# Kernel optimization log

Hardware: AMD Instinct MI355X
Metric: run time of the kernel (lower is better)

## Reference

```python
import jax, jax.numpy as jnp
import numpy as np
from jax import lax

B, T, D, H, S = 256, 512, 256, 512, 8


def setup_inputs() -> dict:
    key = jax.random.key(0)
    ks = jax.random.split(key, 8)
    bound = 1.0 / np.sqrt(H)  # torch LSTMCell/Linear default init scale
    u = lambda k_, shp: jax.random.uniform(k_, shp, jnp.float32, -bound, bound)
    _input = jax.random.normal(ks[0], (B, T, D), jnp.float32)
    h0 = jax.random.normal(ks[1], (B, H), jnp.float32)
    c0 = jax.random.normal(ks[2], (B, H), jnp.float32)
    W_ih = u(ks[3], (4 * H, D))
    W_hh = u(ks[4], (4 * H, H))
    b_ih = u(ks[5], (4 * H,))
    b_hh = u(ks[6], (4 * H,))
    W_lin = u(ks[7], (D, H))
    b_lin = jnp.zeros((D,), jnp.float32)
    # random skip weights per module logic: w1~Bern; w2=1 if w1==0 else Bern; first S steps (1,0)
    rng = np.random.default_rng(0)
    w1 = rng.integers(0, 2, T)
    w2 = np.where(w1 == 0, 1, rng.integers(0, 2, T))
    w1[:S] = 1
    w2[:S] = 0
    return {
        "_input": _input, "h0": h0, "c0": c0,
        "W_ih": W_ih, "W_hh": W_hh, "b_ih": b_ih, "b_hh": b_hh,
        "W_lin": W_lin, "b_lin": b_lin,
        "w1": jnp.asarray(w1, jnp.int32), "w2": jnp.asarray(w2, jnp.int32),
        "time_steps": T, "skip_size": S,
    }


def _lstm_cell(x, h, c, W_ih, W_hh, b_ih, b_hh):
    gates = x @ W_ih.T + b_ih + h @ W_hh.T + b_hh  # [B, 4H]
    i, f, g, o = jnp.split(gates, 4, axis=-1)
    i, f, o = jax.nn.sigmoid(i), jax.nn.sigmoid(f), jax.nn.sigmoid(o)
    c_new = f * c + i * jnp.tanh(g)
    h_new = o * jnp.tanh(c_new)
    return h_new, c_new


def reference(_input, h0, c0, W_ih, W_hh, b_ih, b_hh, W_lin, b_lin, w1, w2, time_steps, skip_size):
    # decoder-mode RSCN: feed previous linear(h) as next input
    buf_h = jnp.repeat(h0[None], skip_size, axis=0)  # FIFO queue as ring buffer [S,B,H]
    buf_c = jnp.repeat(c0[None], skip_size, axis=0)

    def step(carry, xs):
        h_feed, h, c, bh, bc = carry
        w1t, w2t, t = xs
        h_new, c_new = _lstm_cell(h_feed, h, c, W_ih, W_hh, b_ih, b_hh)
        pos = t % skip_size
        skip_h, skip_c = bh[pos], bc[pos]  # queue.get() (oldest)
        bh = bh.at[pos].set(h_new)          # queue.put(new)
        bc = bc.at[pos].set(c_new)
        a = w1t.astype(h_new.dtype)
        b = w2t.astype(h_new.dtype)
        norm = 1.0 / (a + b)
        comb_h = (a * h_new + b * jnp.tanh(skip_h)) * norm
        comb_c = (a * c_new + b * jnp.tanh(skip_c)) * norm
        out = comb_h @ W_lin.T + b_lin  # [B, D]
        return (out, comb_h, comb_c, bh, bc), out

    xs = (w1[:time_steps], w2[:time_steps], jnp.arange(time_steps))
    carry0 = (_input[:, 0, :], h0, c0, buf_h, buf_c)
    (_, h_fin, c_fin, _, _), outs = lax.scan(step, carry0, xs)
    return outs.transpose(1, 0, 2), h_fin, c_fin  # [B,T,D], final (h, c)
```

## Files before the change

### kernel.cpp

```cpp
#include <hip/hip_runtime.h>
#include <math.h>

#define BB 256
#define TT 512
#define DD 256
#define HH 512
#define SS 8
#define G4H 2048
#define BH (BB*HH)
#define OUT_BASE ((size_t)BB*TT*DD)
#define NGRP 16
#define GR 16
#define XSLOT_U32 4096
#define FSTRIDE 16

typedef _Float16 f16;
typedef __attribute__((ext_vector_type(8))) _Float16 f16x8;
typedef __attribute__((ext_vector_type(4))) float    f32x4;

__device__ __forceinline__ float sigm(float x) { return 1.f / (1.f + __expf(-x)); }
__device__ __forceinline__ float ftanh(float x) {
  x = fminf(15.f, fmaxf(-15.f, x));
  float e = __expf(-2.f * x);
  return (1.f - e) / (1.f + e);
}


__global__ __launch_bounds__(256) void prep_wbig16(
    const float* __restrict__ W_ih, const float* __restrict__ W_hh,
    const float* __restrict__ W_lin, f16* __restrict__ Wbig16)
{
  __shared__ float As[64][20];
  __shared__ float Bs[16][68];
  const int n0 = blockIdx.x * 64;
  const int j0 = blockIdx.y * 64;
  const int tid = threadIdx.x;
  const int tn = tid >> 4, tj = tid & 15;
  float acc[4][4] = {};
  for (int k0 = 0; k0 < DD; k0 += 16) {
    { int r = tid >> 2, c = (tid & 3) * 4;
      *(float4*)&As[r][c] = *(const float4*)&W_ih[(size_t)(n0 + r) * DD + k0 + c]; }
    { int r = tid >> 4, c = (tid & 15) * 4;
      *(float4*)&Bs[r][c] = *(const float4*)&W_lin[(size_t)(k0 + r) * HH + j0 + c]; }
    __syncthreads();
    #pragma unroll
    for (int k = 0; k < 16; ++k) {
      float a[4], bv[4];
      #pragma unroll
      for (int i = 0; i < 4; ++i) a[i] = As[tn*4+i][k];
      #pragma unroll
      for (int m = 0; m < 4; ++m) bv[m] = Bs[k][tj*4+m];
      #pragma unroll
      for (int i = 0; i < 4; ++i)
        #pragma unroll
        for (int m = 0; m < 4; ++m)
          acc[i][m] = fmaf(a[i], bv[m], acc[i][m]);
    }
    __syncthreads();
  }
  #pragma unroll
  for (int i = 0; i < 4; ++i) {
    int n = n0 + tn*4 + i;
    #pragma unroll
    for (int m = 0; m < 4; ++m) {
      int j = j0 + tj*4 + m;
      Wbig16[(size_t)n*HH + j] = (f16)(acc[i][m] + W_hh[(size_t)n*HH + j]);
    }
  }
}

__global__ void prep_bias(const float* __restrict__ b_ih, const float* __restrict__ b_hh,
                          const float* __restrict__ W_ih, const float* __restrict__ b_lin,
                          float* __restrict__ bias0, float* __restrict__ bias1)
{
  int n = blockIdx.x * 256 + threadIdx.x;
  float s = b_ih[n] + b_hh[n];
  float d = 0.f;
  for (int k = 0; k < DD; ++k) d = fmaf(W_ih[(size_t)n*DD + k], b_lin[k], d);
  bias0[n] = s;
  bias1[n] = s + d;
}

#define NIH (G4H*DD)
#define NHH (G4H*HH)
__global__ void prep_cvtw(const float* __restrict__ W_ih, const float* __restrict__ W_hh,
                          const float* __restrict__ W_lin,
                          f16* __restrict__ Wih16, f16* __restrict__ Whh16,
                          f16* __restrict__ Wlin16)
{
  int e = blockIdx.x * 256 + threadIdx.x;
  if (e < NIH) Wih16[e] = (f16)W_ih[e];
  else if (e < NIH + NHH) Whh16[e - NIH] = (f16)W_hh[e - NIH];
  else Wlin16[e - NIH - NHH] = (f16)W_lin[e - NIH - NHH];
}

__global__ void prep_init(const float* __restrict__ x0, const float* __restrict__ h0,
                          const float* __restrict__ c0,
                          const int* __restrict__ w1, const int* __restrict__ w2,
                          float* __restrict__ bh, float* __restrict__ bc,
                          f16* __restrict__ x0hi, f16* __restrict__ x0lo,
                          f16* __restrict__ h0hi, f16* __restrict__ h0lo,
                          float4* __restrict__ stepc,
                          int* __restrict__ flags)
{
  int e = blockIdx.x * 256 + threadIdx.x;
  int r = e & (BH - 1);
  bh[e] = h0[r];
  bc[e] = c0[r];
  if (e < BH) {
    float v = h0[e];
    f16 hi = (f16)v;
    h0hi[e] = hi;
    h0lo[e] = (f16)(v - (float)hi);
  }
  if (e < BB*DD) {
    int b = e >> 8, d = e & 255;
    float v = x0[(size_t)b*(TT*DD) + d];
    f16 hi = (f16)v;
    x0hi[e] = hi;
    x0lo[e] = (f16)(v - (float)hi);
  }
  if (e < TT) {
    float a1 = (float)w1[e], a2 = (float)w2[e];
    stepc[e] = make_float4(a1, a2, 1.f / (a1 + a2), 0.f);
  }
  if (e < 4096) flags[e] = 0;
}


__device__ __forceinline__ void stageG(const unsigned* __restrict__ Xs,
                                       f16* lds, int tid) {
  const int lane = tid & 63;
  const int wv = tid >> 6;
  #pragma unroll
  for (int i = 0; i < 2; ++i) {
    int r = wv * 2 + i;
    const char* src = (const char*)Xs + (size_t)r * 1024 +
                      (size_t)((lane ^ r) & 63) * 16;
    __builtin_amdgcn_global_load_lds(
        (const __attribute__((address_space(1))) void*)src,
        (__attribute__((address_space(3))) void*)((char*)lds + r * 1024),
        16, 0, 0x11 );
  }
}

__device__ __forceinline__ void gemm16(const f16x8 (&wA)[16], const f16x8 (&wB)[16],
                                       const f16* lds, int lane,
                                       f32x4& acc0, f32x4& acc1) {
  const int r  = lane & 15;
  const int kc = lane >> 4;
  const int rb = r * 1024;
  #pragma unroll
  for (int ks = 0; ks < 16; ++ks) {
    int u = ks * 4 + kc;
    f16x8 a = *(const f16x8*)((const char*)lds + rb + ((u ^ r) << 4));
    acc0 = __builtin_amdgcn_mfma_f32_16x16x32_f16(a, wA[ks], acc0, 0, 0, 0);
    acc1 = __builtin_amdgcn_mfma_f32_16x16x32_f16(a, wB[ks], acc1, 0, 0, 0);
  }
}

__global__ __launch_bounds__(512, 2) void lstm_persist(
    const f16* __restrict__ x0hi, const f16* __restrict__ x0lo,
    const f16* __restrict__ h0hi, const f16* __restrict__ h0lo,
    const float* __restrict__ c0,
    const f16* __restrict__ Wih16, const f16* __restrict__ Whh16,
    const f16* __restrict__ Wbig16, const f16* __restrict__ Wlin16,
    const float* __restrict__ bias0, const float* __restrict__ bias1,
    const float* __restrict__ b_lin,
    const float4* __restrict__ stepc,
    unsigned* __restrict__ X,
    float* __restrict__ bh, float* __restrict__ bc,
    int* __restrict__ flags,
    float* __restrict__ outp)
{
  __shared__ f16 LdsA[8192];
  __shared__ float gbuf[4096];

  const int tid  = threadIdx.x;
  const int lane = tid & 63;
  const int wv   = tid >> 6;
  const int bid  = blockIdx.x;
  const bool isG = bid < 128;
  const int grp  = isG ? (bid & 15) : (bid - 128);
  const int role = bid >> 4;
  const int b0   = grp * GR;
  const int r16  = lane & 15;
  const int kc   = lane >> 4;
  const int ksel = kc * 8;

  int* gflag = flags + grp * 9 * FSTRIDE;

  int rowA, rowB;
  const f16* wsrc;
  if (isG) {
    rowA = (wv & 3) * 512 + role * 64 + (wv >> 2) * 32 + r16;
    rowB = rowA + 16;
    wsrc = Wbig16;
  } else {
    rowA = wv * 32 + r16;
    rowB = rowA + 16;
    wsrc = Wlin16;
  }
  f16x8 wA[16], wB[16];
  #pragma unroll
  for (int ks = 0; ks < 16; ++ks) {
    wA[ks] = *(const f16x8*)(wsrc + (size_t)rowA * HH + ks * 32 + ksel);
    wB[ks] = *(const f16x8*)(wsrc + (size_t)rowB * HH + ks * 32 + ksel);
  }

  if (isG) {
    int   eidx[2];
    float creg[2];
    const int jl = tid & 63;
    const int jg = role * 64 + jl;
    const float bI = bias1[jg],        bF = bias1[512 + jg];
    const float bG = bias1[1024 + jg], bO = bias1[1536 + jg];
    #pragma unroll
    for (int i = 0; i < 2; ++i) {
      int c = i * 512 + tid;
      int bl = c >> 6;
      eidx[i] = (b0 + bl) * HH + jg;
      creg[i] = c0[eidx[i]];
    }

    for (int t = 0; t < TT; ++t) {
      if (t > 0) {
        if (tid < 8) {
          while (__hip_atomic_load(&gflag[tid * FSTRIDE], __ATOMIC_RELAXED,
                                   __HIP_MEMORY_SCOPE_AGENT) < t) {}
        } else if (tid == 8 && t >= 4) {
          while (__hip_atomic_load(&gflag[8 * FSTRIDE], __ATOMIC_RELAXED,
                                   __HIP_MEMORY_SCOPE_AGENT) < t - 3) {}
        }
        __syncthreads();
        stageG(X + (size_t)(((t - 1) & 3) * NGRP + grp) * XSLOT_U32, LdsA, tid);
      }

      const float4 sc = stepc[t];
      const int pos = t & (SS - 1);
      float shv[2], scv[2];
      #pragma unroll
      for (int i = 0; i < 2; ++i) {
        int bx = pos * BH + eidx[i];
        shv[i] = bh[bx];
        scv[i] = bc[bx];
      }

      f32x4 acc0, acc1;
      #pragma unroll
      for (int i = 0; i < 4; ++i) { acc0[i] = 0.f; acc1[i] = 0.f; }
      if (t == 0) {
        const f16* arh = x0hi + (size_t)(b0 + r16) * DD;
        const f16* arl = x0lo + (size_t)(b0 + r16) * DD;
        const f16* wap = Wih16 + (size_t)rowA * DD;
        const f16* wbp = Wih16 + (size_t)rowB * DD;
        #pragma unroll
        for (int ks = 0; ks < 8; ++ks) {
          int ko = ks * 32 + ksel;
          f16x8 wa = *(const f16x8*)(wap + ko);
          f16x8 wb = *(const f16x8*)(wbp + ko);
          f16x8 ah = *(const f16x8*)(arh + ko);
          f16x8 al = *(const f16x8*)(arl + ko);
          acc0 = __builtin_amdgcn_mfma_f32_16x16x32_f16(ah, wa, acc0, 0, 0, 0);
          acc1 = __builtin_amdgcn_mfma_f32_16x16x32_f16(ah, wb, acc1, 0, 0, 0);
          acc0 = __builtin_amdgcn_mfma_f32_16x16x32_f16(al, wa, acc0, 0, 0, 0);
          acc1 = __builtin_amdgcn_mfma_f32_16x16x32_f16(al, wb, acc1, 0, 0, 0);
        }
        const f16* brh = h0hi + (size_t)(b0 + r16) * HH;
        const f16* brl = h0lo + (size_t)(b0 + r16) * HH;
        const f16* qap = Whh16 + (size_t)rowA * HH;
        const f16* qbp = Whh16 + (size_t)rowB * HH;
        #pragma unroll
        for (int ks = 0; ks < 16; ++ks) {
          int ko = ks * 32 + ksel;
          f16x8 wa = *(const f16x8*)(qap + ko);
          f16x8 wb = *(const f16x8*)(qbp + ko);
          f16x8 ah = *(const f16x8*)(brh + ko);
          f16x8 al = *(const f16x8*)(brl + ko);
          acc0 = __builtin_amdgcn_mfma_f32_16x16x32_f16(ah, wa, acc0, 0, 0, 0);
          acc1 = __builtin_amdgcn_mfma_f32_16x16x32_f16(ah, wb, acc1, 0, 0, 0);
          acc0 = __builtin_amdgcn_mfma_f32_16x16x32_f16(al, wa, acc0, 0, 0, 0);
          acc1 = __builtin_amdgcn_mfma_f32_16x16x32_f16(al, wb, acc1, 0, 0, 0);
        }
      } else {
        __syncthreads();
        gemm16(wA, wB, LdsA, lane, acc0, acc1);
      }

      {
        const int g4 = wv & 3, jh = wv >> 2;
        #pragma unroll
        for (int rg = 0; rg < 4; ++rg) {
          int m  = kc * 4 + rg;
          int j0 = jh * 32 + r16;
          int cs0 = (j0      + 16 * kc) & 63;
          int cs1 = (j0 + 16 + 16 * kc) & 63;
          gbuf[g4 * 1024 + m * 64 + cs0] = acc0[rg];
          gbuf[g4 * 1024 + m * 64 + cs1] = acc1[rg];
        }
      }
      __syncthreads();

      const float a1 = sc.x, a2 = sc.y, nrm = sc.z;
      float baI = bI, baF = bF, baG = bG, baO = bO;
      if (t == 0) {
        baI = bias0[jg];        baF = bias0[512 + jg];
        baG = bias0[1024 + jg]; baO = bias0[1536 + jg];
      }
      unsigned* Xw = X + (size_t)((t & 3) * NGRP + grp) * XSLOT_U32;
      float hnv[2], cnv[2], chv[2];
      #pragma unroll
      for (int i = 0; i < 2; ++i) {
        int c = i * 512 + tid;
        int bl = c >> 6;
        int jj = c & 63;
        int gofs = bl * 64 + ((jj + 16 * (bl >> 2)) & 63);
        float pi = gbuf[gofs]        + baI;
        float pf = gbuf[1024 + gofs] + baF;
        float pg = gbuf[2048 + gofs] + baG;
        float po = gbuf[3072 + gofs] + baO;
        float i_ = sigm(pi), f_ = sigm(pf), o_ = sigm(po), g_ = ftanh(pg);
        float cnew = fmaf(f_, creg[i], i_ * g_);
        float hnew = o_ * ftanh(cnew);
        float ch = (a1 * hnew + a2 * ftanh(shv[i])) * nrm;
        hnv[i] = hnew; cnv[i] = cnew; chv[i] = ch;
        f16 hv = (f16)ch;
        unsigned hb = (unsigned)*(const unsigned short*)&hv;
        unsigned part = (unsigned)__shfl_xor((int)hb, 1);
        if ((tid & 1) == 0)
          __hip_atomic_store(&Xw[bl * 256 + (jg >> 1)], hb | (part << 16),
                             __ATOMIC_RELAXED, __HIP_MEMORY_SCOPE_AGENT);
      }
      __syncthreads();
      if (tid == 0)
        __hip_atomic_store(&gflag[role * FSTRIDE], t + 1, __ATOMIC_RELAXED,
                           __HIP_MEMORY_SCOPE_AGENT);

      #pragma unroll
      for (int i = 0; i < 2; ++i) {
        float cc = (a1 * cnv[i] + a2 * ftanh(scv[i])) * nrm;
        creg[i] = cc;
        int bx = pos * BH + eidx[i];
        bh[bx] = hnv[i];
        bc[bx] = cnv[i];
        if (t == TT - 1) {
          __builtin_nontemporal_store(chv[i], &outp[OUT_BASE + eidx[i]]);
          __builtin_nontemporal_store(cc,     &outp[OUT_BASE + BH + eidx[i]]);
        }
      }
    }
  } else {
    const float bld0 = b_lin[rowA];
    const float bld1 = b_lin[rowB];
    for (int s = 0; s < TT; ++s) {
      if (tid < 8) {
        while (__hip_atomic_load(&gflag[tid * FSTRIDE], __ATOMIC_RELAXED,
                                 __HIP_MEMORY_SCOPE_AGENT) < s + 1) {}
      }
      __syncthreads();
      stageG(X + (size_t)((s & 3) * NGRP + grp) * XSLOT_U32, LdsA, tid);
      __syncthreads();
      if (tid == 0)
        __hip_atomic_store(&gflag[8 * FSTRIDE], s + 1, __ATOMIC_RELAXED,
                           __HIP_MEMORY_SCOPE_AGENT);
      f32x4 acc0, acc1;
      #pragma unroll
      for (int i = 0; i < 4; ++i) { acc0[i] = 0.f; acc1[i] = 0.f; }
      gemm16(wA, wB, LdsA, lane, acc0, acc1);
      const size_t tbase = (size_t)s * DD + wv * 32 + r16;
      #pragma unroll
      for (int rg = 0; rg < 4; ++rg) {
        int m = kc * 4 + rg;
        __builtin_nontemporal_store(acc0[rg] + bld0,
                                    &outp[(size_t)(b0 + m) * (TT*DD) + tbase]);
        __builtin_nontemporal_store(acc1[rg] + bld1,
                                    &outp[(size_t)(b0 + m) * (TT*DD) + tbase + 16]);
      }
      __syncthreads();
    }
  }
}


extern "C" void kernel_launch(void* const* d_in, const int* in_sizes, int n_in,
                              void* d_out, int out_size, void* d_ws, size_t ws_size,
                              hipStream_t stream)
{
  const float* x0    = (const float*)d_in[0];
  const float* h0    = (const float*)d_in[1];
  const float* c0    = (const float*)d_in[2];
  const float* W_ih  = (const float*)d_in[3];
  const float* W_hh  = (const float*)d_in[4];
  const float* b_ih  = (const float*)d_in[5];
  const float* b_hh  = (const float*)d_in[6];
  const float* W_lin = (const float*)d_in[7];
  const float* b_lin = (const float*)d_in[8];
  const int*   w1    = (const int*)d_in[9];
  const int*   w2    = (const int*)d_in[10];

  char* p = (char*)d_ws;
  f16* Wbig16 = (f16*)p;            p += (size_t)G4H*HH*2;
  f16* Wih16  = (f16*)p;            p += (size_t)G4H*DD*2;
  f16* Whh16  = (f16*)p;            p += (size_t)G4H*HH*2;
  f16* Wlin16 = (f16*)p;            p += (size_t)DD*HH*2;
  f16* x0hi   = (f16*)p;            p += (size_t)BB*DD*2;
  f16* x0lo   = (f16*)p;            p += (size_t)BB*DD*2;
  f16* h0hi   = (f16*)p;            p += (size_t)BH*2;
  f16* h0lo   = (f16*)p;            p += (size_t)BH*2;
  unsigned* X = (unsigned*)p;       p += (size_t)4*NGRP*XSLOT_U32*4;
  float* bh   = (float*)p;          p += (size_t)SS*BH*4;
  float* bc   = (float*)p;          p += (size_t)SS*BH*4;
  float* bias0= (float*)p;          p += G4H*4;
  float* bias1= (float*)p;          p += G4H*4;
  float4* stepc = (float4*)p;       p += (size_t)TT*16;
  int*  flags = (int*)p;            p += 4096*4;
  float* outp = (float*)d_out;

  hipLaunchKernelGGL(prep_wbig16, dim3(32, 8), dim3(256), 0, stream,
                     W_ih, W_hh, W_lin, Wbig16);
  hipLaunchKernelGGL(prep_bias, dim3(8), dim3(256), 0, stream,
                     b_ih, b_hh, W_ih, b_lin, bias0, bias1);
  hipLaunchKernelGGL(prep_cvtw, dim3(6656), dim3(256), 0, stream,
                     W_ih, W_hh, W_lin, Wih16, Whh16, Wlin16);
  hipLaunchKernelGGL(prep_init, dim3(4096), dim3(256), 0, stream,
                     x0, h0, c0, w1, w2, bh, bc, x0hi, x0lo, h0hi, h0lo, stepc, flags);

  hipLaunchKernelGGL(lstm_persist, dim3(128 + NGRP), dim3(512), 0, stream,
                     x0hi, x0lo, h0hi, h0lo, c0, Wih16, Whh16, Wbig16, Wlin16,
                     bias0, bias1, b_lin, stepc, X, bh, bc, flags, outp);
}
```

Before: 1.468 ms.

## Read exchanged activations directly from global memory per wave, drop LDS staging

Replaces the block-wide LDS staging of the per-step exchanged X tile, which needed __syncthreads barriers, with per-wave relaxed atomic 64-bit loads straight from global memory into registers that feed the MFMAs. Each wave now spins on the producer flags itself, and the output-projection blocks release their slot flag right after loading. The intent is to shorten the serial per-step critical path by removing block barriers and the LDS round trip. In exchange every wave re-reads the same tile from global/L2, and there is a memory-ordering risk because the loads are relaxed with no acquire fence after the flag spin.

```diff
diff --git a/kernel.cpp b/kernel.cpp
--- a/kernel.cpp
+++ b/kernel.cpp
@@ -128,34 +128,28 @@
 }
 
 
-__device__ __forceinline__ void stageG(const unsigned* __restrict__ Xs,
-                                       f16* lds, int tid) {
-  const int lane = tid & 63;
-  const int wv = tid >> 6;
-  #pragma unroll
-  for (int i = 0; i < 2; ++i) {
-    int r = wv * 2 + i;
-    const char* src = (const char*)Xs + (size_t)r * 1024 +
-                      (size_t)((lane ^ r) & 63) * 16;
-    __builtin_amdgcn_global_load_lds(
-        (const __attribute__((address_space(1))) void*)src,
-        (__attribute__((address_space(3))) void*)((char*)lds + r * 1024),
-        16, 0, 0x11 );
-  }
-}
-
-__device__ __forceinline__ void gemm16(const f16x8 (&wA)[16], const f16x8 (&wB)[16],
-                                       const f16* lds, int lane,
-                                       f32x4& acc0, f32x4& acc1) {
+__device__ __forceinline__ void gemm16D(const f16x8 (&wA)[16], const f16x8 (&wB)[16],
+                                        const unsigned* __restrict__ Xs, int lane,
+                                        f32x4& acc0, f32x4& acc1) {
   const int r  = lane & 15;
   const int kc = lane >> 4;
-  const int rb = r * 1024;
+  const unsigned long long* src =
+      (const unsigned long long*)(Xs + (size_t)r * 256) + kc * 2;
+  unsigned long long v[32];
   #pragma unroll
   for (int ks = 0; ks < 16; ++ks) {
-    int u = ks * 4 + kc;
-    f16x8 a = *(const f16x8*)((const char*)lds + rb + ((u ^ r) << 4));
-    acc0 = __builtin_amdgcn_mfma_f32_16x16x32_f16(a, wA[ks], acc0, 0, 0, 0);
-    acc1 = __builtin_amdgcn_mfma_f32_16x16x32_f16(a, wB[ks], acc1, 0, 0, 0);
+    v[2*ks]   = __hip_atomic_load(src + ks * 8,     __ATOMIC_RELAXED,
+                                  __HIP_MEMORY_SCOPE_AGENT);
+    v[2*ks+1] = __hip_atomic_load(src + ks * 8 + 1, __ATOMIC_RELAXED,
+                                  __HIP_MEMORY_SCOPE_AGENT);
+  }
+  #pragma unroll
+  for (int ks = 0; ks < 16; ++ks) {
+    union { unsigned long long u[2]; f16x8 f; } cvt;
+    cvt.u[0] = v[2*ks];
+    cvt.u[1] = v[2*ks+1];
+    acc0 = __builtin_amdgcn_mfma_f32_16x16x32_f16(cvt.f, wA[ks], acc0, 0, 0, 0);
+    acc1 = __builtin_amdgcn_mfma_f32_16x16x32_f16(cvt.f, wB[ks], acc1, 0, 0, 0);
   }
 }
 
@@ -173,7 +167,6 @@
     int* __restrict__ flags,
     float* __restrict__ outp)
 {
-  __shared__ f16 LdsA[8192];
   __shared__ float gbuf[4096];
 
   const int tid  = threadIdx.x;
@@ -224,18 +217,6 @@
     }
 
     for (int t = 0; t < TT; ++t) {
-      if (t > 0) {
-        if (tid < 8) {
-          while (__hip_atomic_load(&gflag[tid * FSTRIDE], __ATOMIC_RELAXED,
-                                   __HIP_MEMORY_SCOPE_AGENT) < t) {}
-        } else if (tid == 8 && t >= 4) {
-          while (__hip_atomic_load(&gflag[8 * FSTRIDE], __ATOMIC_RELAXED,
-                                   __HIP_MEMORY_SCOPE_AGENT) < t - 3) {}
-        }
-        __syncthreads();
-        stageG(X + (size_t)(((t - 1) & 3) * NGRP + grp) * XSLOT_U32, LdsA, tid);
-      }
-
       const float4 sc = stepc[t];
       const int pos = t & (SS - 1);
       float shv[2], scv[2];
@@ -283,8 +264,16 @@
           acc1 = __builtin_amdgcn_mfma_f32_16x16x32_f16(al, wb, acc1, 0, 0, 0);
         }
       } else {
-        __syncthreads();
-        gemm16(wA, wB, LdsA, lane, acc0, acc1);
+        if (lane < 8) {
+          while (__hip_atomic_load(&gflag[lane * FSTRIDE], __ATOMIC_RELAXED,
+                                   __HIP_MEMORY_SCOPE_AGENT) < t) {}
+        } else if (lane == 8 && t >= 4) {
+          while (__hip_atomic_load(&gflag[8 * FSTRIDE], __ATOMIC_RELAXED,
+                                   __HIP_MEMORY_SCOPE_AGENT) < t - 3) {}
+        }
+        gemm16D(wA, wB,
+                X + (size_t)(((t - 1) & 3) * NGRP + grp) * XSLOT_U32,
+                lane, acc0, acc1);
       }
 
       {
@@ -353,20 +342,20 @@
     const float bld0 = b_lin[rowA];
     const float bld1 = b_lin[rowB];
     for (int s = 0; s < TT; ++s) {
-      if (tid < 8) {
-        while (__hip_atomic_load(&gflag[tid * FSTRIDE], __ATOMIC_RELAXED,
+      if (lane < 8) {
+        while (__hip_atomic_load(&gflag[lane * FSTRIDE], __ATOMIC_RELAXED,
                                  __HIP_MEMORY_SCOPE_AGENT) < s + 1) {}
       }
-      __syncthreads();
-      stageG(X + (size_t)((s & 3) * NGRP + grp) * XSLOT_U32, LdsA, tid);
+      f32x4 acc0, acc1;
+      #pragma unroll
+      for (int i = 0; i < 4; ++i) { acc0[i] = 0.f; acc1[i] = 0.f; }
+      gemm16D(wA, wB,
+              X + (size_t)((s & 3) * NGRP + grp) * XSLOT_U32,
+              lane, acc0, acc1);
       __syncthreads();
       if (tid == 0)
         __hip_atomic_store(&gflag[8 * FSTRIDE], s + 1, __ATOMIC_RELAXED,
                            __HIP_MEMORY_SCOPE_AGENT);
-      f32x4 acc0, acc1;
-      #pragma unroll
-      for (int i = 0; i < 4; ++i) { acc0[i] = 0.f; acc1[i] = 0.f; }
-      gemm16(wA, wB, LdsA, lane, acc0, acc1);
       const size_t tbase = (size_t)s * DD + wv * 32 + r16;
       #pragma unroll
       for (int rg = 0; rg < 4; ++rg) {
@@ -376,7 +365,6 @@
         __builtin_nontemporal_store(acc1[rg] + bld1,
                                     &outp[(size_t)(b0 + m) * (TT*DD) + tbase + 16]);
       }
-      __syncthreads();
     }
   }
 }
```

Measured after the change: 4.674 ms. 218% more time.
